# Performance work log

Hardware: AMD Instinct MI355X
Metric: run time of the kernel (lower is better)

## Reference

```python
import jax, jax.numpy as jnp
import numpy as np

H = 16      # numHeads (== numKeyValueHeads since keyValueHeadsPerHead=1)
D = 128     # headDim


def setup_inputs() -> dict:
    key = jax.random.key(0)
    k1, k2, k3 = jax.random.split(key, 3)
    B, S, dim = 2, 2048, 2048
    x = jax.random.normal(k1, (B, S, dim), dtype=jnp.float32)
    # qkvProj: Linear(dim -> (H + 2*H)*D) without bias; torch Linear weight is [out, in]
    Wqkv = jax.random.normal(k2, ((H + 2 * H) * D, dim), dtype=jnp.float32) * 0.02
    # outProj: Linear(H*D -> dim) without bias
    Wout = jax.random.normal(k3, (dim, H * D), dtype=jnp.float32) * 0.02
    return {"x": x, "Wqkv": Wqkv, "Wout": Wout}


def reference(x, Wqkv, Wout):
    B, S, _ = x.shape
    qkv = jnp.einsum('bsd,ed->bse', x, Wqkv)           # [B, S, 3*H*D]
    qkv = qkv.reshape(B, S, 3 * H, D)
    q = qkv[:, :, :H]                                  # [B, S, H, D]
    k = qkv[:, :, H:2 * H]                             # [B, S, H, D]
    v = qkv[:, :, 2 * H:]                              # [B, S, H, D]
    # explicit QK^T / sqrt(d), softmax in fp32, then @ V (keyValueHeadsPerHead=1
    # collapses the group axis, leaving standard per-head attention)
    logits = jnp.einsum('bqhd,bkhd->bhqk', q, k) * (D ** -0.5)
    w = jax.nn.softmax(logits.astype(jnp.float32), axis=-1).astype(logits.dtype)
    out = jnp.einsum('bhqk,bkhd->bqhd', w, v).reshape(B, S, H * D)
    return jnp.einsum('bse,de->bsd', out, Wout)        # outProj
```

## Files before the change

### kernel.cpp

```cpp
#include <hip/hip_runtime.h>

typedef __bf16 bf16x8 __attribute__((ext_vector_type(8)));
typedef _Float16 f16;
typedef f16 f16x8 __attribute__((ext_vector_type(8)));
typedef float f32x4 __attribute__((ext_vector_type(4)));
typedef unsigned short u16;
typedef u16 u16x4 __attribute__((ext_vector_type(4)));

__device__ __forceinline__ u16 f2bf(float f) {
  unsigned u = __builtin_bit_cast(unsigned, f);
  u += 0x7FFFu + ((u >> 16) & 1u);
  return (u16)(u >> 16);
}

#define GLDS16(g, l) __builtin_amdgcn_global_load_lds(                     \
    (const __attribute__((address_space(1))) unsigned int*)(g),            \
    (__attribute__((address_space(3))) unsigned int*)(l), 16, 0, 0)

__device__ __forceinline__ f32x4 mfma16(bf16x8 a, bf16x8 b, f32x4 c) {
  return __builtin_amdgcn_mfma_f32_16x16x32_bf16(a, b, c, 0, 0, 0);
}
__device__ __forceinline__ f32x4 mfma16h(f16x8 a, f16x8 b, f32x4 c) {
  return __builtin_amdgcn_mfma_f32_16x16x32_f16(a, b, c, 0, 0, 0);
}

__global__ void cvt_all(const float* __restrict__ x, const float* __restrict__ wqkv,
                        const float* __restrict__ wout, u16* __restrict__ xb,
                        u16* __restrict__ wqkvb, u16* __restrict__ woutb, float qscale) {
  int idx = blockIdx.x * blockDim.x + threadIdx.x;
  int stride = gridDim.x * blockDim.x;
  for (int i = idx; i < 6291456; i += stride) {
    const float* src; u16* dst; int j; float sc = 1.0f;
    if (i < 2097152)      { src = x;    dst = xb;    j = i; }
    else if (i < 5242880) { j = i - 2097152; src = wqkv; dst = wqkvb;
                            if (j < 1048576) sc = qscale; }
    else                  { j = i - 5242880; src = wout; dst = woutb; }
    float4 v = ((const float4*)src)[j];
    u16x4 o = { f2bf(v.x * sc), f2bf(v.y * sc), f2bf(v.z * sc), f2bf(v.w * sc) };
    ((u16x4*)dst)[j] = o;
  }
}

__global__ __launch_bounds__(256, 2) void gemm1_qkv(
    const u16* __restrict__ A, const u16* __restrict__ B,
    u16* __restrict__ QK, u16* __restrict__ VT) {
  __shared__ __align__(16) u16 LA[2][8192];
  __shared__ __align__(16) u16 LB[2][12288];
  constexpr int K = 2048;
  const int t = threadIdx.x, lane = t & 63, w = t >> 6;
  const int wm = w >> 1, wn = w & 1;
  const int l15 = lane & 15, lg = lane >> 4;
  const int l7 = l15 & 7;

  const int bid = blockIdx.x;
  const int wg = (bid & 7) * 128 + (bid >> 3);
  const int bx = wg & 31, by = wg >> 5;
  const int m0 = by * 128, n0 = bx * 192;

  const int srow = t >> 3;
  const int schunk = (t & 7) ^ (srow & 7);
  const u16* ga = A + (size_t)(m0 + srow) * K + schunk * 8;
  const u16* gb = B + (size_t)(n0 + srow) * K + schunk * 8;

  f32x4 acc[4][6] = {};

#define STG_A(ch, kt, bfi)                                                 \
    GLDS16(ga + (kt) * 64 + (size_t)(ch) * 32 * K, &LA[bfi][(ch) * 2048] + t * 8)
#define STG_B(ch, kt, bfi)                                                 \
    GLDS16(gb + (kt) * 64 + (size_t)(ch) * 32 * K, &LB[bfi][(ch) * 2048] + t * 8)
#define STG_ALL(kt, bfi) do {                                              \
    STG_A(0, kt, bfi); STG_A(1, kt, bfi); STG_A(2, kt, bfi); STG_A(3, kt, bfi); \
    STG_B(0, kt, bfi); STG_B(1, kt, bfi); STG_B(2, kt, bfi);               \
    STG_B(3, kt, bfi); STG_B(4, kt, bfi); STG_B(5, kt, bfi);               \
  } while (0)

  STG_ALL(0, 0);

#pragma unroll 1
  for (int T = 0; T < 32; ++T) {
    const int p = T & 1, np = p ^ 1;
    if (T < 31) {
      STG_ALL(T + 1, np);
      asm volatile("s_waitcnt vmcnt(10)" ::: "memory");
    } else {
      asm volatile("s_waitcnt vmcnt(0)" ::: "memory");
    }
    __builtin_amdgcn_s_barrier();

    const u16* la = &LA[p][0];
    const u16* lb = &LB[p][0];
    bf16x8 aLo[2][2], aHi[2][2], bLo[2][3], bHi[2][3];
#pragma unroll
    for (int kk = 0; kk < 2; ++kk) {
      const int cp = ((kk * 4 + lg) ^ l7) * 8;
#pragma unroll
      for (int i = 0; i < 2; ++i)
        aLo[kk][i] = *(const bf16x8*)&la[(wm * 64 + i * 16 + l15) * 64 + cp];
#pragma unroll
      for (int j = 0; j < 3; ++j)
        bLo[kk][j] = *(const bf16x8*)&lb[(wn * 96 + j * 16 + l15) * 64 + cp];
#pragma unroll
      for (int j = 0; j < 3; ++j)
        bHi[kk][j] = *(const bf16x8*)&lb[(wn * 96 + 48 + j * 16 + l15) * 64 + cp];
#pragma unroll
      for (int i = 0; i < 2; ++i)
        aHi[kk][i] = *(const bf16x8*)&la[(wm * 64 + 32 + i * 16 + l15) * 64 + cp];
    }
    __builtin_amdgcn_s_setprio(1);
#pragma unroll
    for (int i = 0; i < 2; ++i)
#pragma unroll
      for (int j = 0; j < 3; ++j)
#pragma unroll
        for (int kk = 0; kk < 2; ++kk)
          acc[i][j] = mfma16(aLo[kk][i], bLo[kk][j], acc[i][j]);
#pragma unroll
    for (int i = 0; i < 2; ++i)
#pragma unroll
      for (int j = 0; j < 3; ++j)
#pragma unroll
        for (int kk = 0; kk < 2; ++kk)
          acc[i][3 + j] = mfma16(aLo[kk][i], bHi[kk][j], acc[i][3 + j]);
#pragma unroll
    for (int i = 0; i < 2; ++i)
#pragma unroll
      for (int j = 0; j < 3; ++j)
#pragma unroll
        for (int kk = 0; kk < 2; ++kk)
          acc[2 + i][j] = mfma16(aHi[kk][i], bLo[kk][j], acc[2 + i][j]);
#pragma unroll
    for (int i = 0; i < 2; ++i)
#pragma unroll
      for (int j = 0; j < 3; ++j)
#pragma unroll
        for (int kk = 0; kk < 2; ++kk)
          acc[2 + i][3 + j] = mfma16(aHi[kk][i], bHi[kk][j], acc[2 + i][3 + j]);
    __builtin_amdgcn_s_setprio(0);

    asm volatile("s_waitcnt lgkmcnt(0)" ::: "memory");
    __builtin_amdgcn_s_barrier();
  }
#undef STG_A
#undef STG_B
#undef STG_ALL

  const int rb = m0 + wm * 64 + lg * 4;
  const int cb = n0 + wn * 96 + l15;
#pragma unroll
  for (int i = 0; i < 4; ++i) {
#pragma unroll
    for (int j = 0; j < 6; ++j) {
      const int row0 = rb + i * 16;
      const int col = cb + j * 16;
      if (col < 4096) {
#pragma unroll
        for (int jj = 0; jj < 4; ++jj)
          QK[(size_t)(row0 + jj) * 4096 + col] = f2bf(acc[i][j][jj]);
      } else {
        const int vcol = col - 4096;
        const int bb = row0 >> 11, s = row0 & 2047;
        auto h0 = __builtin_amdgcn_cvt_pkrtz(acc[i][j][0], acc[i][j][1]);
        auto h1 = __builtin_amdgcn_cvt_pkrtz(acc[i][j][2], acc[i][j][3]);
        uint2 pk;
        pk.x = __builtin_bit_cast(unsigned, h0);
        pk.y = __builtin_bit_cast(unsigned, h1);
        *(uint2*)&VT[((size_t)bb * 2048 + vcol) * 2048 + s] = pk;
      }
    }
  }
}

__global__ __launch_bounds__(256, 2) void gemm2_out(
    const u16* __restrict__ A, const u16* __restrict__ B,
    float* __restrict__ C) {
  __shared__ __align__(16) u16 LA[2][8192];
  __shared__ __align__(16) u16 LB[2][8192];
  constexpr int K = 2048, N = 2048;
  const int t = threadIdx.x, lane = t & 63, w = t >> 6;
  const int wm = w >> 1, wn = w & 1;
  const int l15 = lane & 15, lg = lane >> 4;
  const int l7 = l15 & 7;

  const int bid = blockIdx.x;
  const int wg = (bid & 7) * 64 + (bid >> 3);
  const int bx = wg & 15, by = wg >> 4;
  const int m0 = by * 128, n0 = bx * 128;

  const int srow = t >> 3;
  const int schunk = (t & 7) ^ (srow & 7);
  const u16* ga = A + (size_t)(m0 + srow) * K + schunk * 8;
  const u16* gb = B + (size_t)(n0 + srow) * K + schunk * 8;

  f32x4 acc[4][4] = {};

#define STG_A(ch, kt, bfi)                                                 \
    GLDS16(ga + (kt) * 64 + (size_t)(ch) * 32 * K, &LA[bfi][(ch) * 2048] + t * 8)
#define STG_B(ch, kt, bfi)                                                 \
    GLDS16(gb + (kt) * 64 + (size_t)(ch) * 32 * K, &LB[bfi][(ch) * 2048] + t * 8)
#define STG_ALL(kt, bfi) do {                                              \
    STG_A(0, kt, bfi); STG_A(1, kt, bfi); STG_A(2, kt, bfi); STG_A(3, kt, bfi); \
    STG_B(0, kt, bfi); STG_B(1, kt, bfi); STG_B(2, kt, bfi); STG_B(3, kt, bfi); \
  } while (0)

  STG_ALL(0, 0);

#pragma unroll 1
  for (int T = 0; T < 32; ++T) {
    const int p = T & 1, np = p ^ 1;
    if (T < 31) {
      STG_ALL(T + 1, np);
      asm volatile("s_waitcnt vmcnt(8)" ::: "memory");
    } else {
      asm volatile("s_waitcnt vmcnt(0)" ::: "memory");
    }
    __builtin_amdgcn_s_barrier();

    const u16* la = &LA[p][0];
    const u16* lb = &LB[p][0];
    bf16x8 aLo[2][2], aHi[2][2], bLo[2][2], bHi[2][2];
#pragma unroll
    for (int kk = 0; kk < 2; ++kk) {
      const int cp = ((kk * 4 + lg) ^ l7) * 8;
#pragma unroll
      for (int i = 0; i < 2; ++i) {
        aLo[kk][i] = *(const bf16x8*)&la[(wm * 64 + i * 16 + l15) * 64 + cp];
        bLo[kk][i] = *(const bf16x8*)&lb[(wn * 64 + i * 16 + l15) * 64 + cp];
        bHi[kk][i] = *(const bf16x8*)&lb[(wn * 64 + 32 + i * 16 + l15) * 64 + cp];
        aHi[kk][i] = *(const bf16x8*)&la[(wm * 64 + 32 + i * 16 + l15) * 64 + cp];
      }
    }
    __builtin_amdgcn_s_setprio(1);
#pragma unroll
    for (int i = 0; i < 2; ++i)
#pragma unroll
      for (int j = 0; j < 2; ++j)
#pragma unroll
        for (int kk = 0; kk < 2; ++kk)
          acc[i][j] = mfma16(aLo[kk][i], bLo[kk][j], acc[i][j]);
#pragma unroll
    for (int i = 0; i < 2; ++i)
#pragma unroll
      for (int j = 0; j < 2; ++j)
#pragma unroll
        for (int kk = 0; kk < 2; ++kk)
          acc[i][2 + j] = mfma16(aLo[kk][i], bHi[kk][j], acc[i][2 + j]);
#pragma unroll
    for (int i = 0; i < 2; ++i)
#pragma unroll
      for (int j = 0; j < 2; ++j)
#pragma unroll
        for (int kk = 0; kk < 2; ++kk)
          acc[2 + i][j] = mfma16(aHi[kk][i], bLo[kk][j], acc[2 + i][j]);
#pragma unroll
    for (int i = 0; i < 2; ++i)
#pragma unroll
      for (int j = 0; j < 2; ++j)
#pragma unroll
        for (int kk = 0; kk < 2; ++kk)
          acc[2 + i][2 + j] = mfma16(aHi[kk][i], bHi[kk][j], acc[2 + i][2 + j]);
    __builtin_amdgcn_s_setprio(0);

    asm volatile("s_waitcnt lgkmcnt(0)" ::: "memory");
    __builtin_amdgcn_s_barrier();
  }
#undef STG_A
#undef STG_B
#undef STG_ALL

  const int rb = m0 + wm * 64 + lg * 4;
  const int cb = n0 + wn * 64 + l15;
#pragma unroll
  for (int i = 0; i < 4; ++i)
#pragma unroll
    for (int j = 0; j < 4; ++j) {
      const int row0 = rb + i * 16;
      const int col = cb + j * 16;
#pragma unroll
      for (int jj = 0; jj < 4; ++jj)
        C[(size_t)(row0 + jj) * N + col] = acc[i][j][jj];
    }
}

#define PSTRIDE 72
__global__ __launch_bounds__(512, 1) void attn_fwd(
    const u16* __restrict__ qk, const u16* __restrict__ vt, u16* __restrict__ aout) {
  __shared__ __align__(16) u16 Ks[2][64 * 128];
  __shared__ __align__(16) u16 Vs[2][128 * 64];
  __shared__ __align__(16) u16 Pl[8][32 * PSTRIDE];
  const int t = threadIdx.x, lane = t & 63, w = t >> 6;
  const int bh = blockIdx.x;
  const int b = bh >> 4, h = bh & 15;
  const int q0 = blockIdx.y * 256 + w * 32;
  const int l15 = lane & 15, lg = lane >> 4;

  const u16* qp = qk + (size_t)b * 2048 * 4096 + h * 128;
  const u16* kp = qp + 2048;
  const u16* vtp = vt + (size_t)(b * 16 + h) * 128 * 2048;
  u16* op = aout + (size_t)b * 2048 * 2048 + h * 128;

  int ksoff[2], vsoff[2];
#pragma unroll
  for (int rd = 0; rd < 2; ++rd) {
    const int r = rd * 32 + (t >> 4);
    const int c = (t & 15) ^ (r & 15);
    ksoff[rd] = r * 4096 + c * 8;
    const int rv = rd * 64 + (t >> 3);
    const int cv = (t & 7) ^ (rv & 7);
    vsoff[rd] = rv * 2048 + cv * 8;
  }

  bf16x8 qf[2][4];
#pragma unroll
  for (int mi = 0; mi < 2; ++mi)
#pragma unroll
    for (int kd = 0; kd < 4; ++kd)
      qf[mi][kd] = *(const bf16x8*)&qp[(size_t)(q0 + mi * 16 + l15) * 4096 + kd * 32 + lg * 8];

  f32x4 o[2][8] = {};
  f32x4 lacc[2] = {};
  const f16x8 onesf = {f16(1.f), f16(1.f), f16(1.f), f16(1.f),
                       f16(1.f), f16(1.f), f16(1.f), f16(1.f)};
  u16* pw = &Pl[w][0];

#pragma unroll
  for (int rd = 0; rd < 2; ++rd) {
    GLDS16(kp + ksoff[rd], &Ks[0][0] + rd * 4096 + t * 8);
    GLDS16(vtp + vsoff[rd], &Vs[0][0] + rd * 4096 + t * 8);
  }
  __syncthreads();

  auto tile = [&](const u16* ksb, const u16* vsb, u16* kpre, u16* vpre, int nextit) {
    if (nextit < 32) {
      const size_t kt1 = (size_t)nextit * 64;
#pragma unroll
      for (int rd = 0; rd < 2; ++rd) {
        GLDS16(kp + kt1 * 4096 + ksoff[rd], kpre + rd * 4096 + t * 8);
        GLDS16(vtp + kt1 + vsoff[rd], vpre + rd * 4096 + t * 8);
      }
    }
    f32x4 sf[2][4];
    __builtin_amdgcn_s_setprio(1);
#pragma unroll
    for (int ni = 0; ni < 4; ++ni) {
      const int r = ni * 16 + l15;
      bf16x8 kf[4];
#pragma unroll
      for (int kd = 0; kd < 4; ++kd)
        kf[kd] = *(const bf16x8*)&ksb[r * 128 + (((kd * 4 + lg) ^ l15) * 8)];
#pragma unroll
      for (int mi = 0; mi < 2; ++mi) {
        f32x4 s = {0.f, 0.f, 0.f, 0.f};
        s = mfma16(kf[0], qf[mi][0], s);
        s = mfma16(kf[1], qf[mi][1], s);
        s = mfma16(kf[2], qf[mi][2], s);
        s = mfma16(kf[3], qf[mi][3], s);
        sf[mi][ni] = s;
      }
    }
    __builtin_amdgcn_s_setprio(0);

#pragma unroll
    for (int mi = 0; mi < 2; ++mi)
#pragma unroll
      for (int ni = 0; ni < 4; ++ni) {
        float p0 = exp2f(sf[mi][ni][0]);
        float p1 = exp2f(sf[mi][ni][1]);
        float p2 = exp2f(sf[mi][ni][2]);
        float p3 = exp2f(sf[mi][ni][3]);
        auto h0 = __builtin_amdgcn_cvt_pkrtz(p0, p1);
        auto h1 = __builtin_amdgcn_cvt_pkrtz(p2, p3);
        uint2 wv;
        wv.x = __builtin_bit_cast(unsigned, h0);
        wv.y = __builtin_bit_cast(unsigned, h1);
        *(uint2*)&pw[(mi * 16 + l15) * PSTRIDE + ni * 16 + lg * 4] = wv;
      }

    f16x8 pa[2][2];
#pragma unroll
    for (int mi = 0; mi < 2; ++mi)
#pragma unroll
      for (int ks = 0; ks < 2; ++ks)
        pa[mi][ks] = *(const f16x8*)&pw[(mi * 16 + l15) * PSTRIDE + ks * 32 + lg * 8];
    __builtin_amdgcn_s_setprio(1);
#pragma unroll
    for (int mi = 0; mi < 2; ++mi) {
      lacc[mi] = mfma16h(pa[mi][0], onesf, lacc[mi]);
      lacc[mi] = mfma16h(pa[mi][1], onesf, lacc[mi]);
    }
#pragma unroll
    for (int n2 = 0; n2 < 8; ++n2) {
      const int r = n2 * 16 + l15;
      f16x8 vf0 = *(const f16x8*)&vsb[r * 64 + (((0 * 4 + lg) ^ (l15 & 7)) * 8)];
      f16x8 vf1 = *(const f16x8*)&vsb[r * 64 + (((1 * 4 + lg) ^ (l15 & 7)) * 8)];
#pragma unroll
      for (int mi = 0; mi < 2; ++mi) {
        o[mi][n2] = mfma16h(pa[mi][0], vf0, o[mi][n2]);
        o[mi][n2] = mfma16h(pa[mi][1], vf1, o[mi][n2]);
      }
    }
    __builtin_amdgcn_s_setprio(0);
    __syncthreads();
  };

#pragma unroll 1
  for (int it = 0; it < 32; it += 2) {
    tile(&Ks[0][0], &Vs[0][0], &Ks[1][0], &Vs[1][0], it + 1);
    tile(&Ks[1][0], &Vs[1][0], &Ks[0][0], &Vs[0][0], it + 2);
  }

#pragma unroll
  for (int mi = 0; mi < 2; ++mi)
#pragma unroll
    for (int j = 0; j < 4; ++j) {
      float inv = 1.f / lacc[mi][j];
#pragma unroll
      for (int n2 = 0; n2 < 8; ++n2)
        op[(size_t)(q0 + mi * 16 + lg * 4 + j) * 2048 + n2 * 16 + l15] =
            f2bf(o[mi][n2][j] * inv);
    }
}

extern "C" void kernel_launch(void* const* d_in, const int* in_sizes, int n_in,
                              void* d_out, int out_size, void* d_ws, size_t ws_size,
                              hipStream_t stream) {
  const float* x    = (const float*)d_in[0];
  const float* Wqkv = (const float*)d_in[1];
  const float* Wout = (const float*)d_in[2];
  float* out = (float*)d_out;

  u16* ws = (u16*)d_ws;
  u16* xb    = ws;
  u16* wqkvb = ws + 8388608;
  u16* woutb = ws + 20971520;
  u16* qkbuf = ws + 25165824;
  u16* vtbuf = ws + 41943040;
  u16* aout  = xb;

  const float qscale = 0.08838834764831845f * 1.4426950408889634f;

  cvt_all<<<2048, 256, 0, stream>>>(x, Wqkv, Wout, xb, wqkvb, woutb, qscale);

  gemm1_qkv<<<1024, 256, 0, stream>>>(xb, wqkvb, qkbuf, vtbuf);
  attn_fwd<<<dim3(32, 8, 1), 512, 0, stream>>>(qkbuf, vtbuf, aout);
  gemm2_out<<<512, 256, 0, stream>>>(aout, woutb, out);
}
```

Before: 244.9 us.

## Restructure QKV GEMM into 256x256 tiles with 8-wave interleaved load/compute schedule

The QKV projection GEMM moves from 128x192 tiles with 4 waves to 256x256 tiles with 8 waves and one block per CU. It uses a finely interleaved schedule that issues partial global-to-LDS loads between four MFMA quadrant phases, separated by barriers. The larger tile raises arithmetic intensity and the interleaving is meant to hide load latency. The cost is many more barriers and higher register pressure. Separately, the s_setprio hints are removed from the output-projection GEMM.

```diff
diff --git a/kernel.cpp b/kernel.cpp
--- a/kernel.cpp
+++ b/kernel.cpp
@@ -41,123 +41,233 @@
   }
 }
 
-__global__ __launch_bounds__(256, 2) void gemm1_qkv(
+__global__ __launch_bounds__(512, 1) void gemm1_qkv(
     const u16* __restrict__ A, const u16* __restrict__ B,
     u16* __restrict__ QK, u16* __restrict__ VT) {
-  __shared__ __align__(16) u16 LA[2][8192];
-  __shared__ __align__(16) u16 LB[2][12288];
+  __shared__ __align__(16) u16 LA[2][16384];
+  __shared__ __align__(16) u16 LB[2][16384];
   constexpr int K = 2048;
   const int t = threadIdx.x, lane = t & 63, w = t >> 6;
-  const int wm = w >> 1, wn = w & 1;
+  const int wm = w >> 2, wn = w & 3;
   const int l15 = lane & 15, lg = lane >> 4;
   const int l7 = l15 & 7;
 
   const int bid = blockIdx.x;
-  const int wg = (bid & 7) * 128 + (bid >> 3);
-  const int bx = wg & 31, by = wg >> 5;
-  const int m0 = by * 128, n0 = bx * 192;
+  const int wg = (bid & 7) * 48 + (bid >> 3);
+  const int bx = wg % 24, by = wg / 24;
+  const int m0 = by * 256, n0 = bx * 256;
 
   const int srow = t >> 3;
   const int schunk = (t & 7) ^ (srow & 7);
   const u16* ga = A + (size_t)(m0 + srow) * K + schunk * 8;
   const u16* gb = B + (size_t)(n0 + srow) * K + schunk * 8;
 
-  f32x4 acc[4][6] = {};
-
-#define STG_A(ch, kt, bfi)                                                 \
-    GLDS16(ga + (kt) * 64 + (size_t)(ch) * 32 * K, &LA[bfi][(ch) * 2048] + t * 8)
-#define STG_B(ch, kt, bfi)                                                 \
-    GLDS16(gb + (kt) * 64 + (size_t)(ch) * 32 * K, &LB[bfi][(ch) * 2048] + t * 8)
-#define STG_ALL(kt, bfi) do {                                              \
-    STG_A(0, kt, bfi); STG_A(1, kt, bfi); STG_A(2, kt, bfi); STG_A(3, kt, bfi); \
-    STG_B(0, kt, bfi); STG_B(1, kt, bfi); STG_B(2, kt, bfi);               \
-    STG_B(3, kt, bfi); STG_B(4, kt, bfi); STG_B(5, kt, bfi);               \
-  } while (0)
-
-  STG_ALL(0, 0);
+  f32x4 acc[8][4] = {};
+
+#define SA(c, kt, d) GLDS16(ga + (kt) * 64 + (size_t)(c) * 64 * K, &LA[d][(c) * 4096] + t * 8)
+#define SB(c, kt, d) GLDS16(gb + (kt) * 64 + (size_t)(c) * 64 * K, &LB[d][(c) * 4096] + t * 8)
+#define BAR() __builtin_amdgcn_s_barrier()
+#define LGKM0() asm volatile("s_waitcnt lgkmcnt(0)" ::: "memory")
+
+  SA(0, 0, 0); SA(2, 0, 0); SB(0, 0, 0); SB(1, 0, 0); SB(2, 0, 0); SB(3, 0, 0);
+  SA(1, 0, 0); SA(3, 0, 0);
+  SA(0, 1, 1); SA(2, 1, 1); SB(0, 1, 1); SB(1, 1, 1); SB(2, 1, 1); SB(3, 1, 1);
+  asm volatile("s_waitcnt vmcnt(6)" ::: "memory");
+  BAR();
 
 #pragma unroll 1
-  for (int T = 0; T < 32; ++T) {
-    const int p = T & 1, np = p ^ 1;
-    if (T < 31) {
-      STG_ALL(T + 1, np);
-      asm volatile("s_waitcnt vmcnt(10)" ::: "memory");
+  for (int T = 0; T < 16; ++T) {
+    const int k0 = 2 * T, k1 = 2 * T + 1;
+    const bool st = (T < 15);
+    bf16x8 aLo[2][4], aHi[2][4], bLo[2][2], bHi[2][2];
+
+#pragma unroll
+    for (int kk = 0; kk < 2; ++kk) {
+      const int cp = ((kk * 4 + lg) ^ l7) * 8;
+#pragma unroll
+      for (int i = 0; i < 4; ++i)
+        aLo[kk][i] = *(const bf16x8*)&LA[0][(wm * 128 + i * 16 + l15) * 64 + cp];
+#pragma unroll
+      for (int j = 0; j < 2; ++j)
+        bLo[kk][j] = *(const bf16x8*)&LB[0][(wn * 64 + j * 16 + l15) * 64 + cp];
+    }
+    SA(1, k1, 1); SA(3, k1, 1);
+    asm volatile("s_waitcnt lgkmcnt(8)" ::: "memory");
+    BAR(); LGKM0();
+    __builtin_amdgcn_s_setprio(1);
+#pragma unroll
+    for (int i = 0; i < 4; ++i)
+#pragma unroll
+      for (int j = 0; j < 2; ++j)
+#pragma unroll
+        for (int kk = 0; kk < 2; ++kk)
+          acc[i][j] = mfma16(aLo[kk][i], bLo[kk][j], acc[i][j]);
+    __builtin_amdgcn_s_setprio(0);
+    BAR();
+
+#pragma unroll
+    for (int kk = 0; kk < 2; ++kk) {
+      const int cp = ((kk * 4 + lg) ^ l7) * 8;
+#pragma unroll
+      for (int j = 0; j < 2; ++j)
+        bHi[kk][j] = *(const bf16x8*)&LB[0][(wn * 64 + 32 + j * 16 + l15) * 64 + cp];
+    }
+    if (st) { SA(0, k0 + 2, 0); SA(2, k0 + 2, 0); }
+    BAR(); LGKM0();
+    __builtin_amdgcn_s_setprio(1);
+#pragma unroll
+    for (int i = 0; i < 4; ++i)
+#pragma unroll
+      for (int j = 0; j < 2; ++j)
+#pragma unroll
+        for (int kk = 0; kk < 2; ++kk)
+          acc[i][2 + j] = mfma16(aLo[kk][i], bHi[kk][j], acc[i][2 + j]);
+    __builtin_amdgcn_s_setprio(0);
+    BAR();
+
+#pragma unroll
+    for (int kk = 0; kk < 2; ++kk) {
+      const int cp = ((kk * 4 + lg) ^ l7) * 8;
+#pragma unroll
+      for (int i = 0; i < 4; ++i)
+        aHi[kk][i] = *(const bf16x8*)&LA[0][(wm * 128 + 64 + i * 16 + l15) * 64 + cp];
+    }
+    if (st) { SB(0, k0 + 2, 0); SB(1, k0 + 2, 0); }
+    BAR(); LGKM0();
+    __builtin_amdgcn_s_setprio(1);
+#pragma unroll
+    for (int i = 0; i < 4; ++i)
+#pragma unroll
+      for (int j = 0; j < 2; ++j)
+#pragma unroll
+        for (int kk = 0; kk < 2; ++kk)
+          acc[4 + i][j] = mfma16(aHi[kk][i], bLo[kk][j], acc[4 + i][j]);
+    __builtin_amdgcn_s_setprio(0);
+    BAR();
+
+    if (st) {
+      SB(2, k0 + 2, 0); SB(3, k0 + 2, 0);
+      asm volatile("s_waitcnt vmcnt(6)" ::: "memory");
     } else {
       asm volatile("s_waitcnt vmcnt(0)" ::: "memory");
     }
-    __builtin_amdgcn_s_barrier();
-
-    const u16* la = &LA[p][0];
-    const u16* lb = &LB[p][0];
-    bf16x8 aLo[2][2], aHi[2][2], bLo[2][3], bHi[2][3];
-#pragma unroll
-    for (int kk = 0; kk < 2; ++kk) {
-      const int cp = ((kk * 4 + lg) ^ l7) * 8;
-#pragma unroll
-      for (int i = 0; i < 2; ++i)
-        aLo[kk][i] = *(const bf16x8*)&la[(wm * 64 + i * 16 + l15) * 64 + cp];
-#pragma unroll
-      for (int j = 0; j < 3; ++j)
-        bLo[kk][j] = *(const bf16x8*)&lb[(wn * 96 + j * 16 + l15) * 64 + cp];
-#pragma unroll
-      for (int j = 0; j < 3; ++j)
-        bHi[kk][j] = *(const bf16x8*)&lb[(wn * 96 + 48 + j * 16 + l15) * 64 + cp];
-#pragma unroll
-      for (int i = 0; i < 2; ++i)
-        aHi[kk][i] = *(const bf16x8*)&la[(wm * 64 + 32 + i * 16 + l15) * 64 + cp];
-    }
-    __builtin_amdgcn_s_setprio(1);
-#pragma unroll
-    for (int i = 0; i < 2; ++i)
-#pragma unroll
-      for (int j = 0; j < 3; ++j)
+    BAR();
+    __builtin_amdgcn_s_setprio(1);
+#pragma unroll
+    for (int i = 0; i < 4; ++i)
+#pragma unroll
+      for (int j = 0; j < 2; ++j)
+#pragma unroll
+        for (int kk = 0; kk < 2; ++kk)
+          acc[4 + i][2 + j] = mfma16(aHi[kk][i], bHi[kk][j], acc[4 + i][2 + j]);
+    __builtin_amdgcn_s_setprio(0);
+    BAR();
+
+#pragma unroll
+    for (int kk = 0; kk < 2; ++kk) {
+      const int cp = ((kk * 4 + lg) ^ l7) * 8;
+#pragma unroll
+      for (int i = 0; i < 4; ++i)
+        aLo[kk][i] = *(const bf16x8*)&LA[1][(wm * 128 + i * 16 + l15) * 64 + cp];
+#pragma unroll
+      for (int j = 0; j < 2; ++j)
+        bLo[kk][j] = *(const bf16x8*)&LB[1][(wn * 64 + j * 16 + l15) * 64 + cp];
+    }
+    if (st) { SA(1, k0 + 2, 0); SA(3, k0 + 2, 0); }
+    asm volatile("s_waitcnt lgkmcnt(8)" ::: "memory");
+    BAR(); LGKM0();
+    __builtin_amdgcn_s_setprio(1);
+#pragma unroll
+    for (int i = 0; i < 4; ++i)
+#pragma unroll
+      for (int j = 0; j < 2; ++j)
 #pragma unroll
         for (int kk = 0; kk < 2; ++kk)
           acc[i][j] = mfma16(aLo[kk][i], bLo[kk][j], acc[i][j]);
-#pragma unroll
-    for (int i = 0; i < 2; ++i)
-#pragma unroll
-      for (int j = 0; j < 3; ++j)
-#pragma unroll
-        for (int kk = 0; kk < 2; ++kk)
-          acc[i][3 + j] = mfma16(aLo[kk][i], bHi[kk][j], acc[i][3 + j]);
-#pragma unroll
-    for (int i = 0; i < 2; ++i)
-#pragma unroll
-      for (int j = 0; j < 3; ++j)
-#pragma unroll
-        for (int kk = 0; kk < 2; ++kk)
-          acc[2 + i][j] = mfma16(aHi[kk][i], bLo[kk][j], acc[2 + i][j]);
-#pragma unroll
-    for (int i = 0; i < 2; ++i)
-#pragma unroll
-      for (int j = 0; j < 3; ++j)
-#pragma unroll
-        for (int kk = 0; kk < 2; ++kk)
-          acc[2 + i][3 + j] = mfma16(aHi[kk][i], bHi[kk][j], acc[2 + i][3 + j]);
-    __builtin_amdgcn_s_setprio(0);
-
-    asm volatile("s_waitcnt lgkmcnt(0)" ::: "memory");
-    __builtin_amdgcn_s_barrier();
-  }
-#undef STG_A
-#undef STG_B
-#undef STG_ALL
-
-  const int rb = m0 + wm * 64 + lg * 4;
-  const int cb = n0 + wn * 96 + l15;
-#pragma unroll
-  for (int i = 0; i < 4; ++i) {
-#pragma unroll
-    for (int j = 0; j < 6; ++j) {
-      const int row0 = rb + i * 16;
-      const int col = cb + j * 16;
-      if (col < 4096) {
+    __builtin_amdgcn_s_setprio(0);
+    BAR();
+
+#pragma unroll
+    for (int kk = 0; kk < 2; ++kk) {
+      const int cp = ((kk * 4 + lg) ^ l7) * 8;
+#pragma unroll
+      for (int j = 0; j < 2; ++j)
+        bHi[kk][j] = *(const bf16x8*)&LB[1][(wn * 64 + 32 + j * 16 + l15) * 64 + cp];
+    }
+    if (st) { SA(0, k1 + 2, 1); SA(2, k1 + 2, 1); }
+    BAR(); LGKM0();
+    __builtin_amdgcn_s_setprio(1);
+#pragma unroll
+    for (int i = 0; i < 4; ++i)
+#pragma unroll
+      for (int j = 0; j < 2; ++j)
+#pragma unroll
+        for (int kk = 0; kk < 2; ++kk)
+          acc[i][2 + j] = mfma16(aLo[kk][i], bHi[kk][j], acc[i][2 + j]);
+    __builtin_amdgcn_s_setprio(0);
+    BAR();
+
+#pragma unroll
+    for (int kk = 0; kk < 2; ++kk) {
+      const int cp = ((kk * 4 + lg) ^ l7) * 8;
+#pragma unroll
+      for (int i = 0; i < 4; ++i)
+        aHi[kk][i] = *(const bf16x8*)&LA[1][(wm * 128 + 64 + i * 16 + l15) * 64 + cp];
+    }
+    if (st) { SB(0, k1 + 2, 1); SB(1, k1 + 2, 1); }
+    BAR(); LGKM0();
+    __builtin_amdgcn_s_setprio(1);
+#pragma unroll
+    for (int i = 0; i < 4; ++i)
+#pragma unroll
+      for (int j = 0; j < 2; ++j)
+#pragma unroll
+        for (int kk = 0; kk < 2; ++kk)
+          acc[4 + i][j] = mfma16(aHi[kk][i], bLo[kk][j], acc[4 + i][j]);
+    __builtin_amdgcn_s_setprio(0);
+    BAR();
+
+    if (st) {
+      SB(2, k1 + 2, 1); SB(3, k1 + 2, 1);
+      asm volatile("s_waitcnt vmcnt(6)" ::: "memory");
+    }
+    BAR();
+    __builtin_amdgcn_s_setprio(1);
+#pragma unroll
+    for (int i = 0; i < 4; ++i)
+#pragma unroll
+      for (int j = 0; j < 2; ++j)
+#pragma unroll
+        for (int kk = 0; kk < 2; ++kk)
+          acc[4 + i][2 + j] = mfma16(aHi[kk][i], bHi[kk][j], acc[4 + i][2 + j]);
+    __builtin_amdgcn_s_setprio(0);
+    BAR();
+  }
+#undef SA
+#undef SB
+#undef BAR
+#undef LGKM0
+
+  const int rb = m0 + wm * 128 + lg * 4;
+  const int cb0 = wn * 64 + l15;
+  if (n0 < 4096) {
+#pragma unroll
+    for (int i = 0; i < 8; ++i)
+#pragma unroll
+      for (int j = 0; j < 4; ++j) {
+        const int row0 = rb + i * 16;
+        const int col = n0 + cb0 + j * 16;
 #pragma unroll
         for (int jj = 0; jj < 4; ++jj)
           QK[(size_t)(row0 + jj) * 4096 + col] = f2bf(acc[i][j][jj]);
-      } else {
-        const int vcol = col - 4096;
+      }
+  } else {
+#pragma unroll
+    for (int i = 0; i < 8; ++i)
+#pragma unroll
+      for (int j = 0; j < 4; ++j) {
+        const int row0 = rb + i * 16;
+        const int vcol = (n0 - 4096) + cb0 + j * 16;
         const int bb = row0 >> 11, s = row0 & 2047;
         auto h0 = __builtin_amdgcn_cvt_pkrtz(acc[i][j][0], acc[i][j][1]);
         auto h1 = __builtin_amdgcn_cvt_pkrtz(acc[i][j][2], acc[i][j][3]);
@@ -166,7 +276,6 @@
         pk.y = __builtin_bit_cast(unsigned, h1);
         *(uint2*)&VT[((size_t)bb * 2048 + vcol) * 2048 + s] = pk;
       }
-    }
   }
 }
 
@@ -229,7 +338,6 @@
         aHi[kk][i] = *(const bf16x8*)&la[(wm * 64 + 32 + i * 16 + l15) * 64 + cp];
       }
     }
-    __builtin_amdgcn_s_setprio(1);
 #pragma unroll
     for (int i = 0; i < 2; ++i)
 #pragma unroll
@@ -258,7 +366,6 @@
 #pragma unroll
         for (int kk = 0; kk < 2; ++kk)
           acc[2 + i][2 + j] = mfma16(aHi[kk][i], bHi[kk][j], acc[2 + i][2 + j]);
-    __builtin_amdgcn_s_setprio(0);
 
     asm volatile("s_waitcnt lgkmcnt(0)" ::: "memory");
     __builtin_amdgcn_s_barrier();
@@ -440,7 +547,7 @@
 
   cvt_all<<<2048, 256, 0, stream>>>(x, Wqkv, Wout, xb, wqkvb, woutb, qscale);
 
-  gemm1_qkv<<<1024, 256, 0, stream>>>(xb, wqkvb, qkbuf, vtbuf);
+  gemm1_qkv<<<384, 512, 0, stream>>>(xb, wqkvb, qkbuf, vtbuf);
   attn_fwd<<<dim3(32, 8, 1), 512, 0, stream>>>(qkbuf, vtbuf, aout);
   gemm2_out<<<512, 256, 0, stream>>>(aout, woutb, out);
 }
```

After: 256.2 us. 4.6% more time.
